# Performance work log

Hardware: AMD Instinct MI355X
Metric: run time of the kernel (lower is better)

Reference implementation:

```python
import jax, jax.numpy as jnp
import numpy as np

DIM = 1024
NUM_HEADS = 16
HEAD_DIM = DIM // NUM_HEADS


def setup_inputs() -> dict:
    key = jax.random.key(0)
    ks = jax.random.split(key, 9)
    s = 1.0 / np.sqrt(DIM)
    return {
        "x": jax.random.normal(ks[0], (2, 2048, DIM), dtype=jnp.float32),
        "wq": jax.random.uniform(ks[1], (DIM, DIM), jnp.float32, -s, s),
        "bq": jax.random.uniform(ks[2], (DIM,), jnp.float32, -s, s),
        "wk": jax.random.uniform(ks[3], (DIM, DIM), jnp.float32, -s, s),
        "bk": jax.random.uniform(ks[4], (DIM,), jnp.float32, -s, s),
        "wv": jax.random.uniform(ks[5], (DIM, DIM), jnp.float32, -s, s),
        "bv": jax.random.uniform(ks[6], (DIM,), jnp.float32, -s, s),
        "wo": jax.random.uniform(ks[7], (DIM, DIM), jnp.float32, -s, s),
        "bo": jax.random.uniform(ks[8], (DIM,), jnp.float32, -s, s),
    }


def reference(x, wq, bq, wk, bk, wv, bv, wo, bo):
    B, N, D = x.shape
    H, Hd = NUM_HEADS, HEAD_DIM
    # projections; weights stored as (in, out) so x @ w matches torch Linear(x) with w = W.T
    q = (x @ wq + bq).reshape(B, N, H, Hd).transpose(0, 2, 1, 3)  # [B,H,N,Hd]
    k = (x @ wk + bk).reshape(B, N, H, Hd).transpose(0, 2, 1, 3)
    v = (x @ wv + bv).reshape(B, N, H, Hd).transpose(0, 2, 1, 3)
    scale = 1.0 / np.sqrt(Hd).astype(np.float32)
    scores = jnp.einsum("bhqd,bhkd->bhqk", q, k) * scale  # [B,H,N,N]
    attn = jax.nn.softmax(scores, axis=-1)
    # dropout is identity in eval mode (reference baseline)
    out = jnp.einsum("bhqk,bhkd->bhqd", attn, v)  # [B,H,N,Hd]
    out = out.transpose(0, 2, 1, 3).reshape(B, N, D)
    return out @ wo + bo
```

## Files before the change

### kernel.cpp

```cpp
#include <hip/hip_runtime.h>

typedef __attribute__((ext_vector_type(8))) short short8;
typedef __attribute__((ext_vector_type(4))) short short4v;
typedef __attribute__((ext_vector_type(8))) unsigned short u16x8;
typedef __attribute__((ext_vector_type(4))) float f32x4;

__device__ inline unsigned short f2bf(float f) {
  union { float f; unsigned int u; } v; v.f = f;
  unsigned int r = v.u + 0x7FFFu + ((v.u >> 16) & 1u);
  return (unsigned short)(r >> 16);
}

__device__ inline unsigned short f2bf_trunc(float f) {
  union { float f; unsigned int u; } v; v.f = f;
  return (unsigned short)(v.u >> 16);
}

__device__ inline void gload_lds16(const void* g, void* l) {
  __builtin_amdgcn_global_load_lds(
      (const __attribute__((address_space(1))) unsigned int*)g,
      (__attribute__((address_space(3))) unsigned int*)l, 16, 0, 0);
}


__global__ void cvt_bf16(const float4* __restrict__ in, ushort4* __restrict__ out) {
  const int i = blockIdx.x * blockDim.x + threadIdx.x;
  float4 v = in[i];
  ushort4 o;
  o.x = f2bf(v.x); o.y = f2bf(v.y); o.z = f2bf(v.z); o.w = f2bf(v.w);
  out[i] = o;
}

__global__ __launch_bounds__(256) void cvt_wT_all(
    const float* __restrict__ wq, const float* __restrict__ wk,
    const float* __restrict__ wv, const float* __restrict__ wo,
    unsigned short* __restrict__ wqkvT, unsigned short* __restrict__ woT) {
  const int z = blockIdx.z;
  const float* w = (z == 0) ? wq : (z == 1) ? wk : (z == 2) ? wv : wo;
  unsigned short* dst = (z < 3) ? (wqkvT + (size_t)z * 1024 * 1024) : woT;
  const float scale = (z == 0) ? 0.18033688011f : 1.0f;
  __shared__ float t[32][33];
  const int k0 = blockIdx.x * 32;
  const int n0 = blockIdx.y * 32;
  const int tx = threadIdx.x & 31, ty = threadIdx.x >> 5;
#pragma unroll
  for (int i = 0; i < 32; i += 8)
    t[ty + i][tx] = w[(size_t)(k0 + ty + i) * 1024 + n0 + tx];
  __syncthreads();
#pragma unroll
  for (int i = 0; i < 32; i += 8)
    dst[(size_t)(n0 + ty + i) * 1024 + k0 + tx] = f2bf(t[tx][ty + i] * scale);
}

__global__ void pack_bias(const float* __restrict__ bq, const float* __restrict__ bk,
                          const float* __restrict__ bv, float* __restrict__ out) {
  const int i = blockIdx.x * 256 + threadIdx.x;
  float v;
  if (i < 1024) v = bq[i] * 0.18033688011f;
  else if (i < 2048) v = bk[i - 1024];
  else v = bv[i - 2048];
  out[i] = v;
}


template <typename OutT>
__global__ __launch_bounds__(256) void gemm_bt(
    const unsigned short* __restrict__ A, const unsigned short* __restrict__ Bt,
    const float* __restrict__ bias, OutT* __restrict__ C,
    int K, int ldc) {
  __shared__ unsigned short As[128 * 32];
  __shared__ unsigned short Bs[128 * 32];
  const int tid = threadIdx.x;
  const int lane = tid & 63;
  const int wave = tid >> 6;
  const int wm = (wave >> 1) * 64;
  const int wn = (wave & 1) * 64;
  const long bm = (long)blockIdx.x * 128;
  const long bn = (long)blockIdx.y * 128;

  const int sr = tid >> 2;
  const int sc = (tid & 3) * 8;
  const unsigned short* Ag0 = A + (bm + sr) * (long)K + sc;
  const unsigned short* Ag1 = A + (bm + 64 + sr) * (long)K + sc;
  const unsigned short* Bg0 = Bt + (bn + sr) * (long)K + sc;
  const unsigned short* Bg1 = Bt + (bn + 64 + sr) * (long)K + sc;
  unsigned short* As0 = &As[tid * 8];
  unsigned short* As1 = &As[2048 + tid * 8];
  unsigned short* Bs0 = &Bs[tid * 8];
  unsigned short* Bs1 = &Bs[2048 + tid * 8];

  f32x4 acc[4][4] = {};

  const int fr = lane & 15;
  const int fk = (lane >> 4) * 8;

  for (int kt = 0; kt < K; kt += 32) {
    gload_lds16(Ag0, As0);
    gload_lds16(Ag1, As1);
    gload_lds16(Bg0, Bs0);
    gload_lds16(Bg1, Bs1);
    Ag0 += 32; Ag1 += 32; Bg0 += 32; Bg1 += 32;
    __syncthreads();
    short8 af[4], bfv[4];
#pragma unroll
    for (int i = 0; i < 4; i++) af[i] = *(const short8*)&As[(wm + i * 16 + fr) * 32 + fk];
#pragma unroll
    for (int j = 0; j < 4; j++) bfv[j] = *(const short8*)&Bs[(wn + j * 16 + fr) * 32 + fk];
#pragma unroll
    for (int i = 0; i < 4; i++)
#pragma unroll
      for (int j = 0; j < 4; j++)
        acc[i][j] = __builtin_amdgcn_mfma_f32_16x16x32_bf16(af[i], bfv[j], acc[i][j], 0, 0, 0);
    __syncthreads();
  }

  const int crow = (lane >> 4) * 4;
  const int ccol = lane & 15;
#pragma unroll
  for (int j = 0; j < 4; j++) {
    const long col = bn + wn + j * 16 + ccol;
    const float bv = bias[col];
#pragma unroll
    for (int i = 0; i < 4; i++) {
#pragma unroll
      for (int r = 0; r < 4; r++) {
        const long row = bm + wm + i * 16 + crow + r;
        const float val = acc[i][j][r] + bv;
        if constexpr (__is_same(OutT, float)) C[row * ldc + col] = val;
        else                                  C[row * ldc + col] = f2bf(val);
      }
    }
  }
}


__global__ __launch_bounds__(512, 2) void gemm256(
    const unsigned short* __restrict__ A, const unsigned short* __restrict__ Bt,
    const float* __restrict__ bias, unsigned short* __restrict__ C, int ldc) {
  constexpr int K = 1024;
  __shared__ unsigned short Sab[2][2][16384];
  const int tid = threadIdx.x;
  const int lane = tid & 63;
  const int w = tid >> 6;
  const int wr = w >> 2, wc = w & 3;
  const long bm = (long)blockIdx.x * 256;
  const long bn = (long)blockIdx.y * 256;
  const int fr = lane & 15, fg = lane >> 4;

  const int srow = tid >> 3;
  const int kch = tid & 7;

  auto stage = [&](int o, int buf, int tk, int h) {
#pragma unroll
    for (int l = 0; l < 2; ++l) {
      const int rih = l * 64 + srow;
      const unsigned short* src = (o ? Bt : A) +
          ((o ? bn : bm) + h * 128 + rih) * (long)K + tk * 64 + ((kch ^ (rih & 7)) * 8);
      gload_lds16(src, &Sab[buf][o][h * 8192 + (l * 512 + tid) * 8]);
    }
  };

  f32x4 acc[8][4] = {};

  stage(0, 0, 0, 0); stage(0, 0, 0, 1);
  stage(1, 0, 0, 0); stage(1, 0, 0, 1);
  stage(1, 1, 1, 0); stage(1, 1, 1, 1);
  asm volatile("s_waitcnt vmcnt(4)" ::: "memory");
  __builtin_amdgcn_s_barrier();

  for (int it = 0; it < 8; ++it) {
    const int T = 2 * it;
    const int tkA = (T + 2 < 15) ? T + 2 : 15;
    const int tkB3 = (T + 3 < 15) ? T + 3 : 15;
#pragma unroll
    for (int half = 0; half < 2; ++half) {
      const int b = half;
      short8 bfr[4][2];
      short8 afr[2][2];
#pragma unroll
      for (int g = 0; g < 4; ++g) {
        if (g == 0) {
#pragma unroll
          for (int nj = 0; nj < 4; ++nj)
#pragma unroll
            for (int kc = 0; kc < 2; ++kc) {
              const int r = wc * 64 + nj * 16 + fr;
              bfr[nj][kc] = *(const short8*)&Sab[b][1][r * 64 + ((kc * 4 + fg) ^ (r & 7)) * 8];
            }
        }
#pragma unroll
        for (int mil = 0; mil < 2; ++mil)
#pragma unroll
          for (int kc = 0; kc < 2; ++kc) {
            const int r = wr * 128 + (2 * g + mil) * 16 + fr;
            afr[mil][kc] = *(const short8*)&Sab[b][0][r * 64 + ((kc * 4 + fg) ^ (r & 7)) * 8];
          }
        if (half == 0) {
          if (g == 0)      { stage(0, 1, T + 1, 0); stage(0, 1, T + 1, 1); }
          else if (g == 1) { stage(1, 0, tkA, 0); }
          else if (g == 2) { stage(1, 0, tkA, 1); }
        } else {
          if (g == 0)      { stage(0, 0, tkA, 0); stage(0, 0, tkA, 1); }
          else if (g == 1) { stage(1, 1, tkB3, 0); }
          else if (g == 2) { stage(1, 1, tkB3, 1); }
        }
        __builtin_amdgcn_s_barrier();
        asm volatile("s_waitcnt lgkmcnt(0)" ::: "memory");
        __builtin_amdgcn_sched_barrier(0);
        __builtin_amdgcn_s_setprio(1);
#pragma unroll
        for (int mil = 0; mil < 2; ++mil)
#pragma unroll
          for (int nj = 0; nj < 4; ++nj)
#pragma unroll
            for (int kc = 0; kc < 2; ++kc)
              acc[2 * g + mil][nj] = __builtin_amdgcn_mfma_f32_16x16x32_bf16(
                  afr[mil][kc], bfr[nj][kc], acc[2 * g + mil][nj], 0, 0, 0);
        __builtin_amdgcn_s_setprio(0);
        if (g == 3) asm volatile("s_waitcnt vmcnt(4)" ::: "memory");
        __builtin_amdgcn_s_barrier();
      }
    }
  }

  const int crow = fg * 4;
  const int ccol = fr;
#pragma unroll
  for (int nj = 0; nj < 4; ++nj) {
    const long col = bn + wc * 64 + nj * 16 + ccol;
    const float bv = bias[col];
#pragma unroll
    for (int mi = 0; mi < 8; ++mi)
#pragma unroll
      for (int r = 0; r < 4; ++r) {
        const long row = bm + wr * 128 + mi * 16 + crow + r;
        C[row * ldc + col] = f2bf(acc[mi][nj][r] + bv);
      }
  }
}


#define TRRD(d, o) asm volatile("ds_read_b64_tr_b16 %0, %1 offset:" o \
                                : "=v"(d) : "v"(vtr) : "memory")
#define LGKM(n) asm volatile("s_waitcnt lgkmcnt(" #n ")" ::: "memory")

__global__ __launch_bounds__(256, 4) void attn_fwd(
    const unsigned short* __restrict__ qkv, unsigned short* __restrict__ out) {
  __shared__ unsigned short Ks[2 * 4096];
  __shared__ unsigned short Vs[2 * 4096];
  __shared__ unsigned short Ps[64 * 64];
  const int tid = threadIdx.x;
  const int lane = tid & 63;
  const int w = tid >> 6;
  const int qh = w >> 1, kh = w & 1;

  const int xcd = blockIdx.x & 7, slot = blockIdx.x >> 3;
  const int pair = xcd * 4 + (slot >> 5);
  const int qtile = slot & 31;
  const int h = pair & 15, b = pair >> 4;
  const long rowbase = (long)b * 2048;
  const int hq = h * 64;
  const int fr = lane & 15;
  const int fg = lane >> 4;
  const int fk = fg * 8;
  const int q0 = qtile * 64 + qh * 32;

  short8 qf[2][2];
#pragma unroll
  for (int qi = 0; qi < 2; qi++) {
    const long qr = rowbase + q0 + qi * 16 + fr;
    qf[qi][0] = *(const short8*)&qkv[qr * 3072 + hq + fk];
    qf[qi][1] = *(const short8*)&qkv[qr * 3072 + hq + 32 + fk];
  }

  const int kr0 = tid >> 3, kr1 = 32 + (tid >> 3);
  const unsigned short* Kg0 = &qkv[(rowbase + kr0) * 3072 + 1024 + hq + (((tid & 7) ^ (kr0 & 7)) * 8)];
  const unsigned short* Kg1 = &qkv[(rowbase + kr1) * 3072 + 1024 + hq + (((tid & 7) ^ (kr1 & 7)) * 8)];
  const int vkv0 = ((tid >> 3) & 3) * 8 + ((tid >> 5) & 1) * 4 + ((tid >> 1) & 3);
  const int vd0 = ((tid >> 6) & 3) * 16 + (tid & 1) * 8;
  const unsigned short* Vg0 = &qkv[(rowbase + vkv0) * 3072 + 2048 + hq + vd0];
  const unsigned short* Vg1 = &qkv[(rowbase + vkv0 + 32) * 3072 + 2048 + hq + vd0];

  auto stage = [&](int buf) {
    gload_lds16(Kg0, &Ks[buf * 4096 + tid * 8]);
    gload_lds16(Kg1, &Ks[buf * 4096 + 2048 + tid * 8]);
    gload_lds16(Vg0, &Vs[buf * 4096 + tid * 8]);
    gload_lds16(Vg1, &Vs[buf * 4096 + 2048 + tid * 8]);
    Kg0 += 64 * 3072; Kg1 += 64 * 3072; Vg0 += 64 * 3072; Vg1 += 64 * 3072;
  };

  short8 onesv;
#pragma unroll
  for (int e = 0; e < 8; e++) onesv[e] = (short)0x3F80;

  f32x4 o[2][4] = {};
  f32x4 s_acc[2] = {};
  float m_[2][4];
#pragma unroll
  for (int qi = 0; qi < 2; qi++)
#pragma unroll
    for (int r = 0; r < 4; r++) m_[qi][r] = -1e30f;

  stage(0);
  __syncthreads();

  for (int t = 0; t < 32; t++) {
    const int cur = t & 1;
    if (t < 31) stage(cur ^ 1);

    f32x4 sa[2][2];
    __builtin_amdgcn_s_setprio(1);
#pragma unroll
    for (int n = 0; n < 2; n++) {
      const int row = kh * 32 + n * 16 + fr;
      const short8 kf0 = *(const short8*)&Ks[cur * 4096 + ((row * 64 + fk) ^ ((fr & 7) << 3))];
      const short8 kf1 = *(const short8*)&Ks[cur * 4096 + ((row * 64 + 32 + fk) ^ ((fr & 7) << 3))];
#pragma unroll
      for (int qi = 0; qi < 2; qi++) {
        f32x4 z = {0.f, 0.f, 0.f, 0.f};
        z = __builtin_amdgcn_mfma_f32_16x16x32_bf16(qf[qi][0], kf0, z, 0, 0, 0);
        sa[qi][n] = __builtin_amdgcn_mfma_f32_16x16x32_bf16(qf[qi][1], kf1, z, 0, 0, 0);
      }
    }
    __builtin_amdgcn_s_setprio(0);

    float lmax;
    {
      float a0 = fmaxf(fmaxf(sa[0][0][0], sa[0][0][1]), fmaxf(sa[0][0][2], sa[0][0][3]));
      float a1 = fmaxf(fmaxf(sa[0][1][0], sa[0][1][1]), fmaxf(sa[0][1][2], sa[0][1][3]));
      float a2 = fmaxf(fmaxf(sa[1][0][0], sa[1][0][1]), fmaxf(sa[1][0][2], sa[1][0][3]));
      float a3 = fmaxf(fmaxf(sa[1][1][0], sa[1][1][1]), fmaxf(sa[1][1][2], sa[1][1][3]));
      lmax = fmaxf(fmaxf(a0, a1), fmaxf(a2, a3));
    }
    float mmin = m_[0][0];
#pragma unroll
    for (int qi = 0; qi < 2; qi++)
#pragma unroll
      for (int r = 0; r < 4; r++) mmin = fminf(mmin, m_[qi][r]);
    if (__any(lmax - mmin > 8.f)) {
#pragma unroll
      for (int qi = 0; qi < 2; qi++) {
        float mx[4];
#pragma unroll
        for (int r = 0; r < 4; r++) mx[r] = fmaxf(sa[qi][0][r], sa[qi][1][r]);
#pragma unroll
        for (int r = 0; r < 4; r++) {
          for (int off = 1; off < 16; off <<= 1) mx[r] = fmaxf(mx[r], __shfl_xor(mx[r], off));
        }
#pragma unroll
        for (int r = 0; r < 4; r++) {
          const float nm = fmaxf(m_[qi][r], mx[r]);
          const float fac = __builtin_amdgcn_exp2f(m_[qi][r] - nm);
          m_[qi][r] = nm;
          s_acc[qi][r] *= fac;
#pragma unroll
          for (int dj = 0; dj < 4; dj++) o[qi][dj][r] *= fac;
        }
      }
    }

#pragma unroll
    for (int qi = 0; qi < 2; qi++)
#pragma unroll
      for (int n = 0; n < 2; n++)
#pragma unroll
        for (int r = 0; r < 4; r++) {
          const float p = __builtin_amdgcn_exp2f(sa[qi][n][r] - m_[qi][r]);
          const int prow = qh * 32 + qi * 16 + fg * 4 + r;
          const int pcol = (kh * 32 + n * 16 + fr) ^ ((prow & 7) << 3);
          Ps[prow * 64 + pcol] = f2bf_trunc(p);
        }

    short8 pa[2];
#pragma unroll
    for (int qi = 0; qi < 2; qi++) {
      const int rrow = qh * 32 + qi * 16 + fr;
      pa[qi] = *(const short8*)&Ps[rrow * 64 + (((kh * 4 + fg) ^ (fr & 7)) * 8)];
    }

    s_acc[0] = __builtin_amdgcn_mfma_f32_16x16x32_bf16(pa[0], onesv, s_acc[0], 0, 0, 0);
    s_acc[1] = __builtin_amdgcn_mfma_f32_16x16x32_bf16(pa[1], onesv, s_acc[1], 0, 0, 0);

    const __attribute__((address_space(3))) unsigned short* vtr =
        (const __attribute__((address_space(3))) unsigned short*)&Vs[0] +
        cur * 4096 + kh * 2048 + lane * 4;
    short4v v0[4], v1[4];
    TRRD(v0[0], "0");    TRRD(v1[0], "512");
    TRRD(v0[1], "1024"); TRRD(v1[1], "1536");
    TRRD(v0[2], "2048"); TRRD(v1[2], "2560");
    TRRD(v0[3], "3072"); TRRD(v1[3], "3584");

    __builtin_amdgcn_s_setprio(1);
    LGKM(6); __builtin_amdgcn_sched_barrier(0);
    {
      short8 vf = __builtin_shufflevector(v0[0], v1[0], 0, 1, 2, 3, 4, 5, 6, 7);
      o[0][0] = __builtin_amdgcn_mfma_f32_16x16x32_bf16(pa[0], vf, o[0][0], 0, 0, 0);
      o[1][0] = __builtin_amdgcn_mfma_f32_16x16x32_bf16(pa[1], vf, o[1][0], 0, 0, 0);
    }
    LGKM(4); __builtin_amdgcn_sched_barrier(0);
    {
      short8 vf = __builtin_shufflevector(v0[1], v1[1], 0, 1, 2, 3, 4, 5, 6, 7);
      o[0][1] = __builtin_amdgcn_mfma_f32_16x16x32_bf16(pa[0], vf, o[0][1], 0, 0, 0);
      o[1][1] = __builtin_amdgcn_mfma_f32_16x16x32_bf16(pa[1], vf, o[1][1], 0, 0, 0);
    }
    LGKM(2); __builtin_amdgcn_sched_barrier(0);
    {
      short8 vf = __builtin_shufflevector(v0[2], v1[2], 0, 1, 2, 3, 4, 5, 6, 7);
      o[0][2] = __builtin_amdgcn_mfma_f32_16x16x32_bf16(pa[0], vf, o[0][2], 0, 0, 0);
      o[1][2] = __builtin_amdgcn_mfma_f32_16x16x32_bf16(pa[1], vf, o[1][2], 0, 0, 0);
    }
    LGKM(0); __builtin_amdgcn_sched_barrier(0);
    {
      short8 vf = __builtin_shufflevector(v0[3], v1[3], 0, 1, 2, 3, 4, 5, 6, 7);
      o[0][3] = __builtin_amdgcn_mfma_f32_16x16x32_bf16(pa[0], vf, o[0][3], 0, 0, 0);
      o[1][3] = __builtin_amdgcn_mfma_f32_16x16x32_bf16(pa[1], vf, o[1][3], 0, 0, 0);
    }
    __builtin_amdgcn_s_setprio(0);
    __syncthreads();
  }

  float* mo = (float*)&Ks[0];
  float* ms = (float*)&Vs[0];
  if (kh == 1) {
#pragma unroll
    for (int qi = 0; qi < 2; qi++)
#pragma unroll
      for (int dj = 0; dj < 4; dj++)
#pragma unroll
        for (int r = 0; r < 4; r++)
          mo[qh * 2048 + (qi * 16 + dj * 4 + r) * 64 + lane] = o[qi][dj][r];
#pragma unroll
    for (int qi = 0; qi < 2; qi++)
#pragma unroll
      for (int r = 0; r < 4; r++) {
        ms[qh * 1024 + (qi * 4 + r) * 64 + lane] = m_[qi][r];
        ms[qh * 1024 + (8 + qi * 4 + r) * 64 + lane] = s_acc[qi][r];
      }
  }
  __syncthreads();
  if (kh == 0) {
    float f0[2][4], f1[2][4], rs[2][4];
#pragma unroll
    for (int qi = 0; qi < 2; qi++)
#pragma unroll
      for (int r = 0; r < 4; r++) {
        const float m1 = ms[qh * 1024 + (qi * 4 + r) * 64 + lane];
        const float s1 = ms[qh * 1024 + (8 + qi * 4 + r) * 64 + lane];
        const float m0 = m_[qi][r], s0 = s_acc[qi][r];
        const float mstar = fmaxf(m0, m1);
        f0[qi][r] = __builtin_amdgcn_exp2f(m0 - mstar);
        f1[qi][r] = __builtin_amdgcn_exp2f(m1 - mstar);
        rs[qi][r] = __builtin_amdgcn_rcpf(s0 * f0[qi][r] + s1 * f1[qi][r]);
      }
#pragma unroll
    for (int qi = 0; qi < 2; qi++)
#pragma unroll
      for (int dj = 0; dj < 4; dj++)
#pragma unroll
        for (int r = 0; r < 4; r++) {
          const float o1 = mo[qh * 2048 + (qi * 16 + dj * 4 + r) * 64 + lane];
          const float val = (o[qi][dj][r] * f0[qi][r] + o1 * f1[qi][r]) * rs[qi][r];
          const long row = rowbase + q0 + qi * 16 + fg * 4 + r;
          out[row * 1024 + hq + dj * 16 + fr] = f2bf(val);
        }
  }
}


extern "C" void kernel_launch(void* const* d_in, const int* in_sizes, int n_in,
                              void* d_out, int out_size, void* d_ws, size_t ws_size,
                              hipStream_t stream) {
  const float* x  = (const float*)d_in[0];
  const float* wq = (const float*)d_in[1];
  const float* bq = (const float*)d_in[2];
  const float* wk = (const float*)d_in[3];
  const float* bk = (const float*)d_in[4];
  const float* wv = (const float*)d_in[5];
  const float* bv = (const float*)d_in[6];
  const float* wo = (const float*)d_in[7];
  const float* bo = (const float*)d_in[8];

  char* ws = (char*)d_ws;
  unsigned short* xb    = (unsigned short*)(ws);
  unsigned short* wqkvT = (unsigned short*)(ws + (8ull  << 20));
  unsigned short* woT   = (unsigned short*)(ws + (14ull << 20));
  float*          bqkv  = (float*)         (ws + (16ull << 20));
  unsigned short* qkv   = (unsigned short*)(ws + (17ull << 20));
  unsigned short* attn  = (unsigned short*)(ws + (41ull << 20));

  cvt_bf16<<<4096, 256, 0, stream>>>((const float4*)x, (ushort4*)xb);
  cvt_wT_all<<<dim3(32, 32, 4), 256, 0, stream>>>(wq, wk, wv, wo, wqkvT, woT);
  pack_bias<<<12, 256, 0, stream>>>(bq, bk, bv, bqkv);

  gemm256<<<dim3(16, 12), 512, 0, stream>>>(xb, wqkvT, bqkv, qkv, 3072);

  attn_fwd<<<1024, 256, 0, stream>>>(qkv, attn);

  gemm_bt<float><<<dim3(32, 8), 256, 0, stream>>>(attn, woT, bo, (float*)d_out, 1024, 1024);
}
```

Before: 135.0 us.

## Keep softmax probabilities in registers via transposed QK MFMA and merge prep kernels

The attention kernel now computes S^T (K as the A operand), so each lane holds the scores for one query column. The exponentiated probabilities can then be packed to bf16 with v_cvt_pk_bf16_f32 and fed straight to the PV MFMA without the Ps shared-memory round trip. Row sums are taken with shuffles instead of a ones-vector MFMA, and max/sum state shrinks to one value per query tile. Freeing the LDS allows a higher occupancy bound (5). Separately, the three preprocessing kernels are merged into one launch; the risks are added shuffle cost for rescaling and more register pressure under the new launch bound.

```diff
diff --git a/kernel.cpp b/kernel.cpp
--- a/kernel.cpp
+++ b/kernel.cpp
@@ -2,7 +2,6 @@
 
 typedef __attribute__((ext_vector_type(8))) short short8;
 typedef __attribute__((ext_vector_type(4))) short short4v;
-typedef __attribute__((ext_vector_type(8))) unsigned short u16x8;
 typedef __attribute__((ext_vector_type(4))) float f32x4;
 
 __device__ inline unsigned short f2bf(float f) {
@@ -11,9 +10,10 @@
   return (unsigned short)(r >> 16);
 }
 
-__device__ inline unsigned short f2bf_trunc(float f) {
-  union { float f; unsigned int u; } v; v.f = f;
-  return (unsigned short)(v.u >> 16);
+__device__ inline unsigned cvtpk_bf16(float lo, float hi) {
+  unsigned r;
+  asm("v_cvt_pk_bf16_f32 %0, %1, %2" : "=v"(r) : "v"(lo), "v"(hi));
+  return r;
 }
 
 __device__ inline void gload_lds16(const void* g, void* l) {
@@ -23,43 +23,46 @@
 }
 
 
-__global__ void cvt_bf16(const float4* __restrict__ in, ushort4* __restrict__ out) {
-  const int i = blockIdx.x * blockDim.x + threadIdx.x;
-  float4 v = in[i];
-  ushort4 o;
-  o.x = f2bf(v.x); o.y = f2bf(v.y); o.z = f2bf(v.z); o.w = f2bf(v.w);
-  out[i] = o;
-}
-
-__global__ __launch_bounds__(256) void cvt_wT_all(
+__global__ __launch_bounds__(256) void prep(
+    const float* __restrict__ x,
     const float* __restrict__ wq, const float* __restrict__ wk,
     const float* __restrict__ wv, const float* __restrict__ wo,
-    unsigned short* __restrict__ wqkvT, unsigned short* __restrict__ woT) {
-  const int z = blockIdx.z;
-  const float* w = (z == 0) ? wq : (z == 1) ? wk : (z == 2) ? wv : wo;
-  unsigned short* dst = (z < 3) ? (wqkvT + (size_t)z * 1024 * 1024) : woT;
-  const float scale = (z == 0) ? 0.18033688011f : 1.0f;
-  __shared__ float t[32][33];
-  const int k0 = blockIdx.x * 32;
-  const int n0 = blockIdx.y * 32;
-  const int tx = threadIdx.x & 31, ty = threadIdx.x >> 5;
-#pragma unroll
-  for (int i = 0; i < 32; i += 8)
-    t[ty + i][tx] = w[(size_t)(k0 + ty + i) * 1024 + n0 + tx];
-  __syncthreads();
-#pragma unroll
-  for (int i = 0; i < 32; i += 8)
-    dst[(size_t)(n0 + ty + i) * 1024 + k0 + tx] = f2bf(t[tx][ty + i] * scale);
-}
-
-__global__ void pack_bias(const float* __restrict__ bq, const float* __restrict__ bk,
-                          const float* __restrict__ bv, float* __restrict__ out) {
-  const int i = blockIdx.x * 256 + threadIdx.x;
-  float v;
-  if (i < 1024) v = bq[i] * 0.18033688011f;
-  else if (i < 2048) v = bk[i - 1024];
-  else v = bv[i - 2048];
-  out[i] = v;
+    const float* __restrict__ bq, const float* __restrict__ bk,
+    const float* __restrict__ bv,
+    unsigned short* __restrict__ xb, unsigned short* __restrict__ wqkvT,
+    unsigned short* __restrict__ woT, float* __restrict__ bqkv) {
+  const int bid = blockIdx.x;
+  if (bid < 4096) {
+    const int i = bid * 256 + threadIdx.x;
+    float4 v = ((const float4*)x)[i];
+    ushort4 o;
+    o.x = f2bf(v.x); o.y = f2bf(v.y); o.z = f2bf(v.z); o.w = f2bf(v.w);
+    ((ushort4*)xb)[i] = o;
+  } else if (bid < 8192) {
+    const int u = bid - 4096;
+    const int z = u >> 10, rem = u & 1023;
+    const float* w = (z == 0) ? wq : (z == 1) ? wk : (z == 2) ? wv : wo;
+    unsigned short* dst = (z < 3) ? (wqkvT + (size_t)z * 1024 * 1024) : woT;
+    const float scale = (z == 0) ? 0.18033688011f : 1.0f;
+    __shared__ float t[32][33];
+    const int k0 = (rem & 31) * 32;
+    const int n0 = (rem >> 5) * 32;
+    const int tx = threadIdx.x & 31, ty = threadIdx.x >> 5;
+#pragma unroll
+    for (int i = 0; i < 32; i += 8)
+      t[ty + i][tx] = w[(size_t)(k0 + ty + i) * 1024 + n0 + tx];
+    __syncthreads();
+#pragma unroll
+    for (int i = 0; i < 32; i += 8)
+      dst[(size_t)(n0 + ty + i) * 1024 + k0 + tx] = f2bf(t[tx][ty + i] * scale);
+  } else {
+    const int i = (bid - 8192) * 256 + threadIdx.x;
+    float v;
+    if (i < 1024) v = bq[i] * 0.18033688011f;
+    else if (i < 2048) v = bk[i - 1024];
+    else v = bv[i - 2048];
+    bqkv[i] = v;
+  }
 }
 
 
@@ -244,11 +247,10 @@
                                 : "=v"(d) : "v"(vtr) : "memory")
 #define LGKM(n) asm volatile("s_waitcnt lgkmcnt(" #n ")" ::: "memory")
 
-__global__ __launch_bounds__(256, 4) void attn_fwd(
+__global__ __launch_bounds__(256, 5) void attn_fwd(
     const unsigned short* __restrict__ qkv, unsigned short* __restrict__ out) {
   __shared__ unsigned short Ks[2 * 4096];
   __shared__ unsigned short Vs[2 * 4096];
-  __shared__ unsigned short Ps[64 * 64];
   const int tid = threadIdx.x;
   const int lane = tid & 63;
   const int w = tid >> 6;
@@ -289,17 +291,11 @@
     Kg0 += 64 * 3072; Kg1 += 64 * 3072; Vg0 += 64 * 3072; Vg1 += 64 * 3072;
   };
 
-  short8 onesv;
-#pragma unroll
-  for (int e = 0; e < 8; e++) onesv[e] = (short)0x3F80;
-
   f32x4 o[2][4] = {};
-  f32x4 s_acc[2] = {};
-  float m_[2][4];
-#pragma unroll
-  for (int qi = 0; qi < 2; qi++)
-#pragma unroll
-    for (int r = 0; r < 4; r++) m_[qi][r] = -1e30f;
+  float m_[2] = {-1e30f, -1e30f};
+  float s_[2] = {0.f, 0.f};
+
+  const int krowbase = kh * 32 + (fr >> 2) * 8 + (fr & 3);
 
   stage(0);
   __syncthreads();
@@ -312,74 +308,63 @@
     __builtin_amdgcn_s_setprio(1);
 #pragma unroll
     for (int n = 0; n < 2; n++) {
-      const int row = kh * 32 + n * 16 + fr;
-      const short8 kf0 = *(const short8*)&Ks[cur * 4096 + ((row * 64 + fk) ^ ((fr & 7) << 3))];
-      const short8 kf1 = *(const short8*)&Ks[cur * 4096 + ((row * 64 + 32 + fk) ^ ((fr & 7) << 3))];
+      const int row = krowbase + n * 4;
+      const short8 kf0 = *(const short8*)&Ks[cur * 4096 + ((row * 64 + fk) ^ ((row & 7) << 3))];
+      const short8 kf1 = *(const short8*)&Ks[cur * 4096 + ((row * 64 + 32 + fk) ^ ((row & 7) << 3))];
 #pragma unroll
       for (int qi = 0; qi < 2; qi++) {
         f32x4 z = {0.f, 0.f, 0.f, 0.f};
-        z = __builtin_amdgcn_mfma_f32_16x16x32_bf16(qf[qi][0], kf0, z, 0, 0, 0);
-        sa[qi][n] = __builtin_amdgcn_mfma_f32_16x16x32_bf16(qf[qi][1], kf1, z, 0, 0, 0);
+        z = __builtin_amdgcn_mfma_f32_16x16x32_bf16(kf0, qf[qi][0], z, 0, 0, 0);
+        sa[qi][n] = __builtin_amdgcn_mfma_f32_16x16x32_bf16(kf1, qf[qi][1], z, 0, 0, 0);
       }
     }
     __builtin_amdgcn_s_setprio(0);
 
-    float lmax;
-    {
-      float a0 = fmaxf(fmaxf(sa[0][0][0], sa[0][0][1]), fmaxf(sa[0][0][2], sa[0][0][3]));
-      float a1 = fmaxf(fmaxf(sa[0][1][0], sa[0][1][1]), fmaxf(sa[0][1][2], sa[0][1][3]));
-      float a2 = fmaxf(fmaxf(sa[1][0][0], sa[1][0][1]), fmaxf(sa[1][0][2], sa[1][0][3]));
-      float a3 = fmaxf(fmaxf(sa[1][1][0], sa[1][1][1]), fmaxf(sa[1][1][2], sa[1][1][3]));
-      lmax = fmaxf(fmaxf(a0, a1), fmaxf(a2, a3));
-    }
-    float mmin = m_[0][0];
+    float lmax[2];
 #pragma unroll
     for (int qi = 0; qi < 2; qi++)
-#pragma unroll
-      for (int r = 0; r < 4; r++) mmin = fminf(mmin, m_[qi][r]);
-    if (__any(lmax - mmin > 8.f)) {
+      lmax[qi] = fmaxf(fmaxf(fmaxf(sa[qi][0][0], sa[qi][0][1]), fmaxf(sa[qi][0][2], sa[qi][0][3])),
+                       fmaxf(fmaxf(sa[qi][1][0], sa[qi][1][1]), fmaxf(sa[qi][1][2], sa[qi][1][3])));
+    if (__any(fmaxf(lmax[0] - m_[0], lmax[1] - m_[1]) > 8.f)) {
 #pragma unroll
       for (int qi = 0; qi < 2; qi++) {
-        float mx[4];
-#pragma unroll
-        for (int r = 0; r < 4; r++) mx[r] = fmaxf(sa[qi][0][r], sa[qi][1][r]);
-#pragma unroll
-        for (int r = 0; r < 4; r++) {
-          for (int off = 1; off < 16; off <<= 1) mx[r] = fmaxf(mx[r], __shfl_xor(mx[r], off));
-        }
-#pragma unroll
-        for (int r = 0; r < 4; r++) {
-          const float nm = fmaxf(m_[qi][r], mx[r]);
-          const float fac = __builtin_amdgcn_exp2f(m_[qi][r] - nm);
-          m_[qi][r] = nm;
-          s_acc[qi][r] *= fac;
-#pragma unroll
-          for (int dj = 0; dj < 4; dj++) o[qi][dj][r] *= fac;
-        }
-      }
-    }
-
-#pragma unroll
-    for (int qi = 0; qi < 2; qi++)
+        float mx = lmax[qi];
+        mx = fmaxf(mx, __shfl_xor(mx, 16));
+        mx = fmaxf(mx, __shfl_xor(mx, 32));
+        const float nm = fmaxf(m_[qi], mx);
+        const float fac = __builtin_amdgcn_exp2f(m_[qi] - nm);
+        m_[qi] = nm;
+        s_[qi] *= fac;
+        float facp[4];
+#pragma unroll
+        for (int r = 0; r < 4; r++) facp[r] = __shfl(fac, fg * 4 + r);
+#pragma unroll
+        for (int dj = 0; dj < 4; dj++)
+#pragma unroll
+          for (int r = 0; r < 4; r++) o[qi][dj][r] *= facp[r];
+      }
+    }
+
+    short8 pa[2];
+#pragma unroll
+    for (int qi = 0; qi < 2; qi++) {
+      float p[8];
 #pragma unroll
       for (int n = 0; n < 2; n++)
 #pragma unroll
-        for (int r = 0; r < 4; r++) {
-          const float p = __builtin_amdgcn_exp2f(sa[qi][n][r] - m_[qi][r]);
-          const int prow = qh * 32 + qi * 16 + fg * 4 + r;
-          const int pcol = (kh * 32 + n * 16 + fr) ^ ((prow & 7) << 3);
-          Ps[prow * 64 + pcol] = f2bf_trunc(p);
-        }
-
-    short8 pa[2];
-#pragma unroll
-    for (int qi = 0; qi < 2; qi++) {
-      const int rrow = qh * 32 + qi * 16 + fr;
-      pa[qi] = *(const short8*)&Ps[rrow * 64 + (((kh * 4 + fg) ^ (fr & 7)) * 8)];
-    }
-
-    s_acc[0] = __builtin_amdgcn_mfma_f32_16x16x32_bf16(pa[0], onesv, s_acc[0], 0, 0, 0);
-    s_acc[1] = __builtin_amdgcn_mfma_f32_16x16x32_bf16(pa[1], onesv, s_acc[1], 0, 0, 0);
+        for (int r = 0; r < 4; r++)
+          p[n * 4 + r] = __builtin_amdgcn_exp2f(sa[qi][n][r] - m_[qi]);
+      float sl = ((p[0] + p[1]) + (p[2] + p[3])) + ((p[4] + p[5]) + (p[6] + p[7]));
+      sl += __shfl_xor(sl, 16);
+      sl += __shfl_xor(sl, 32);
+      s_[qi] += sl;
+      union { unsigned u[4]; short8 v; } pk;
+      pk.u[0] = cvtpk_bf16(p[0], p[1]);
+      pk.u[1] = cvtpk_bf16(p[2], p[3]);
+      pk.u[2] = cvtpk_bf16(p[4], p[5]);
+      pk.u[3] = cvtpk_bf16(p[6], p[7]);
+      pa[qi] = pk.v;
+    }
 
     const __attribute__((address_space(3))) unsigned short* vtr =
         (const __attribute__((address_space(3))) unsigned short*)&Vs[0] +
@@ -421,6 +406,7 @@
 
   float* mo = (float*)&Ks[0];
   float* ms = (float*)&Vs[0];
+  __syncthreads();
   if (kh == 1) {
 #pragma unroll
     for (int qi = 0; qi < 2; qi++)
@@ -428,41 +414,42 @@
       for (int dj = 0; dj < 4; dj++)
 #pragma unroll
         for (int r = 0; r < 4; r++)
-          mo[qh * 2048 + (qi * 16 + dj * 4 + r) * 64 + lane] = o[qi][dj][r];
-#pragma unroll
-    for (int qi = 0; qi < 2; qi++)
-#pragma unroll
-      for (int r = 0; r < 4; r++) {
-        ms[qh * 1024 + (qi * 4 + r) * 64 + lane] = m_[qi][r];
-        ms[qh * 1024 + (8 + qi * 4 + r) * 64 + lane] = s_acc[qi][r];
-      }
+          mo[(qh * 32 + qi * 16 + dj * 4 + r) * 64 + lane] = o[qi][dj][r];
+  }
+  if (fg == 0) {
+#pragma unroll
+    for (int qi = 0; qi < 2; qi++) {
+      ms[(((kh * 2 + qh) * 2 + qi) * 2 + 0) * 16 + fr] = m_[qi];
+      ms[(((kh * 2 + qh) * 2 + qi) * 2 + 1) * 16 + fr] = s_[qi];
+    }
   }
   __syncthreads();
   if (kh == 0) {
-    float f0[2][4], f1[2][4], rs[2][4];
-#pragma unroll
-    for (int qi = 0; qi < 2; qi++)
+#pragma unroll
+    for (int qi = 0; qi < 2; qi++) {
+      float f0[4], f1[4], rs[4];
 #pragma unroll
       for (int r = 0; r < 4; r++) {
-        const float m1 = ms[qh * 1024 + (qi * 4 + r) * 64 + lane];
-        const float s1 = ms[qh * 1024 + (8 + qi * 4 + r) * 64 + lane];
-        const float m0 = m_[qi][r], s0 = s_acc[qi][r];
+        const int qp = fg * 4 + r;
+        const float m0 = ms[(((0 * 2 + qh) * 2 + qi) * 2 + 0) * 16 + qp];
+        const float s0 = ms[(((0 * 2 + qh) * 2 + qi) * 2 + 1) * 16 + qp];
+        const float m1 = ms[(((1 * 2 + qh) * 2 + qi) * 2 + 0) * 16 + qp];
+        const float s1 = ms[(((1 * 2 + qh) * 2 + qi) * 2 + 1) * 16 + qp];
         const float mstar = fmaxf(m0, m1);
-        f0[qi][r] = __builtin_amdgcn_exp2f(m0 - mstar);
-        f1[qi][r] = __builtin_amdgcn_exp2f(m1 - mstar);
-        rs[qi][r] = __builtin_amdgcn_rcpf(s0 * f0[qi][r] + s1 * f1[qi][r]);
-      }
-#pragma unroll
-    for (int qi = 0; qi < 2; qi++)
+        f0[r] = __builtin_amdgcn_exp2f(m0 - mstar);
+        f1[r] = __builtin_amdgcn_exp2f(m1 - mstar);
+        rs[r] = __builtin_amdgcn_rcpf(s0 * f0[r] + s1 * f1[r]);
+      }
 #pragma unroll
       for (int dj = 0; dj < 4; dj++)
 #pragma unroll
         for (int r = 0; r < 4; r++) {
-          const float o1 = mo[qh * 2048 + (qi * 16 + dj * 4 + r) * 64 + lane];
-          const float val = (o[qi][dj][r] * f0[qi][r] + o1 * f1[qi][r]) * rs[qi][r];
+          const float o1 = mo[(qh * 32 + qi * 16 + dj * 4 + r) * 64 + lane];
+          const float val = (o[qi][dj][r] * f0[r] + o1 * f1[r]) * rs[r];
           const long row = rowbase + q0 + qi * 16 + fg * 4 + r;
           out[row * 1024 + hq + dj * 16 + fr] = f2bf(val);
         }
+    }
   }
 }
 
@@ -488,9 +475,7 @@
   unsigned short* qkv   = (unsigned short*)(ws + (17ull << 20));
   unsigned short* attn  = (unsigned short*)(ws + (41ull << 20));
 
-  cvt_bf16<<<4096, 256, 0, stream>>>((const float4*)x, (ushort4*)xb);
-  cvt_wT_all<<<dim3(32, 32, 4), 256, 0, stream>>>(wq, wk, wv, wo, wqkvT, woT);
-  pack_bias<<<12, 256, 0, stream>>>(bq, bk, bv, bqkv);
+  prep<<<8204, 256, 0, stream>>>(x, wq, wk, wv, wo, bq, bk, bv, xb, wqkvT, woT, bqkv);
 
   gemm256<<<dim3(16, 12), 512, 0, stream>>>(xb, wqkvT, bqkv, qkv, 3072);
 
```

Result: faster. 127.6 us (-5.5%).
